# Optimization experiments

Measured on AMD Instinct MI355X. Metric: run time of the kernel, lower is better.

Reference implementation:

```python
import jax, jax.numpy as jnp
import numpy as np

B, S, HID, NH = 2, 2048, 1024, 16
HD = HID // NH
SCALE = HD ** -0.5


def elu_plus_one(x):
    return jax.nn.elu(x) + 1.0


def setup_inputs() -> dict:
    key = jax.random.key(0)
    ks = jax.random.split(key, 8)
    w_scale = 0.02  # keep logits in a sane range
    return {
        "hidden_states": jax.random.normal(ks[0], (B, S, HID), jnp.float32),
        "wq": jax.random.normal(ks[1], (HID, HID), jnp.float32) * w_scale,
        "wk": jax.random.normal(ks[2], (HID, HID), jnp.float32) * w_scale,
        "wv": jax.random.normal(ks[3], (HID, HID), jnp.float32) * w_scale,
        "wo": jax.random.normal(ks[4], (HID, HID), jnp.float32) * w_scale,
        "beta": jax.random.normal(ks[5], (NH,), jnp.float32),
        "memory": jax.random.normal(ks[6], (NH, HD, HD), jnp.float32),
        "memory_norm": jax.random.uniform(ks[7], (NH, HD), jnp.float32),
    }


def reference(hidden_states, wq, wk, wv, wo, beta, memory, memory_norm):
    b, s, _ = hidden_states.shape
    # nn.Linear(bias=False): x @ W^T; weights stored [out, in]
    def proj(x, w):
        return jnp.einsum("bsh,oh->bso", x, w).reshape(b, s, NH, HD).transpose(0, 2, 1, 3)

    q = proj(hidden_states, wq)  # [B,H,S,D]
    k = proj(hidden_states, wk)
    v = proj(hidden_states, wv)

    # local causal softmax attention (materializes [B,H,S,S] as the original does)
    scores = jnp.einsum("bhsd,bhtd->bhst", q, k) * SCALE
    causal_mask = jnp.triu(jnp.full((s, s), -jnp.inf, dtype=scores.dtype), k=1)
    attn = jax.nn.softmax(scores + causal_mask, axis=-1)
    a_local = jnp.einsum("bhst,bhtd->bhsd", attn, v)

    # compressive memory retrieval: sigma(Q) @ M / (sigma(Q) @ z)
    sigma_q = elu_plus_one(q)
    a_mem_unnorm = jnp.einsum("bhsd,hde->bhse", sigma_q, memory)
    norm = jnp.clip(jnp.einsum("bhsd,hd->bhs", sigma_q, memory_norm), 1e-6, None)
    a_mem = a_mem_unnorm / norm[..., None]

    gate = jax.nn.sigmoid(beta).reshape(1, NH, 1, 1)
    combined = gate * a_mem + (1.0 - gate) * a_local  # [B,H,S,D]
    combined = combined.transpose(0, 2, 1, 3).reshape(b, s, HID)
    return jnp.einsum("bsh,oh->bso", combined, wo)
```

## Files before the change

kernel.cpp:

```cpp
#include <hip/hip_runtime.h>
#include <stdint.h>

#define LOG2E 1.4426950408889634f

typedef __attribute__((ext_vector_type(8))) __bf16 bf16x8;
typedef __attribute__((ext_vector_type(4))) __bf16 bf16x4;
typedef __attribute__((ext_vector_type(4))) float f32x4;

__device__ inline void gll16(const void* g, void* l) {
  __builtin_amdgcn_global_load_lds(
      (const __attribute__((address_space(1))) void*)g,
      (__attribute__((address_space(3))) void*)l, 16, 0, 0);
}

__global__ __launch_bounds__(256) void cvt_all(
    const float* __restrict__ hs, const float* __restrict__ wq,
    const float* __restrict__ wk, const float* __restrict__ wv,
    const float* __restrict__ wo,
    __bf16* __restrict__ hsb, __bf16* __restrict__ wqb, __bf16* __restrict__ wkb,
    __bf16* __restrict__ wvb, __bf16* __restrict__ wob) {
  int bid = blockIdx.x;
  const float* s; __bf16* d; int i;
  if (bid < 4096) { s = hs; d = hsb; i = bid * 256 + threadIdx.x; }
  else {
    int seg = (bid - 4096) >> 10;
    i = ((bid - 4096) & 1023) * 256 + threadIdx.x;
    s = seg == 0 ? wq : seg == 1 ? wk : seg == 2 ? wv : wo;
    d = seg == 0 ? wqb : seg == 1 ? wkb : seg == 2 ? wvb : wob;
  }
  float4 v = ((const float4*)s)[i];
  bf16x4 o;
  o[0] = (__bf16)v.x; o[1] = (__bf16)v.y; o[2] = (__bf16)v.z; o[3] = (__bf16)v.w;
  *(bf16x4*)&d[(size_t)i * 4] = o;
}

#define KSCALE 0.18033688011112042f
__global__ __launch_bounds__(256, 3) void qkv_gemm(
    const __bf16* __restrict__ hsb, const __bf16* __restrict__ wqb,
    const __bf16* __restrict__ wkb, const __bf16* __restrict__ wvb,
    __bf16* __restrict__ qbuf, __bf16* __restrict__ kbuf,
    __bf16* __restrict__ vtb) {
  constexpr int K = 1024;
  __shared__ __align__(16) __bf16 lta[128 * 32];
  __shared__ __align__(16) __bf16 ltb[128 * 32];
  const int bid = blockIdx.x;
  const int z = bid >> 8, r = bid & 255;
  const __bf16 *A, *Bt;
  int m0, n0;
  if (z < 2) {
    A = hsb; Bt = z ? wkb : wqb;
    m0 = (r & 31) * 128; n0 = (r >> 5) * 128;
  } else {
    A = wvb; Bt = hsb;
    m0 = (r & 7) * 128; n0 = (r >> 3) * 128;
  }
  const int tid = threadIdx.x;
  const int w = tid >> 6, l = tid & 63;
  const int lg = l >> 4, lr = l & 15;
  const int wm = (w >> 1) * 64, wn = (w & 1) * 64;
  f32x4 acc[4][4] = {};
  const int srow = w * 16 + (l >> 2);
  const int scol = (l & 3) * 8;
  const __bf16* ga = A + (size_t)(m0 + srow) * K + scol;
  const __bf16* gb = Bt + (size_t)(n0 + srow) * K + scol;
  __bf16* la = &lta[(size_t)w * 16 * 32];
  __bf16* lb = &ltb[(size_t)w * 16 * 32];
  for (int k0 = 0; k0 < K; k0 += 32) {
    __syncthreads();
    gll16(ga + k0, la);
    gll16(ga + 64 * K + k0, la + 64 * 32);
    gll16(gb + k0, lb);
    gll16(gb + 64 * K + k0, lb + 64 * 32);
    __syncthreads();
    bf16x8 af[4], bfr[4];
#pragma unroll
    for (int i = 0; i < 4; ++i) {
      af[i]  = *(const bf16x8*)&lta[(wm + i * 16 + lr) * 32 + lg * 8];
      bfr[i] = *(const bf16x8*)&ltb[(wn + i * 16 + lr) * 32 + lg * 8];
    }
#pragma unroll
    for (int i = 0; i < 4; ++i)
#pragma unroll
      for (int j = 0; j < 4; ++j)
        acc[i][j] = __builtin_amdgcn_mfma_f32_16x16x32_bf16(af[i], bfr[j], acc[i][j], 0, 0, 0);
  }
#pragma unroll
  for (int i = 0; i < 4; ++i)
#pragma unroll
    for (int j = 0; j < 4; ++j)
#pragma unroll
      for (int rr = 0; rr < 4; ++rr) {
        int gm = m0 + wm + i * 16 + lg * 4 + rr;
        int gn = n0 + wn + j * 16 + lr;
        float v = acc[i][j][rr];
        if (z < 2) {
          int bb = gm >> 11, s = gm & 2047, hh = gn >> 6, d = gn & 63;
          __bf16* dst = z ? kbuf : qbuf;
          if (z) v *= KSCALE;
          dst[(((size_t)bb * 16 + hh) * 2048 + s) * 64 + d] = (__bf16)v;
        } else {
          int bb = gn >> 11, s = gn & 2047, hh = gm >> 6, d = gm & 63;
          vtb[(((size_t)bb * 16 + hh) * 64 + d) * 2048 + s] = (__bf16)v;
        }
      }
}

__global__ __launch_bounds__(256, 2) void gemm_out(const __bf16* __restrict__ A,
                                                   const __bf16* __restrict__ Bt,
                                                   float* __restrict__ C,
                                                   int M, int N) {
  constexpr int K = 1024;
  __shared__ __align__(16) __bf16 lta[128 * 32];
  __shared__ __align__(16) __bf16 ltb[64 * 32];
  const int tid = threadIdx.x;
  const int w = tid >> 6, l = tid & 63;
  const int lg = l >> 4, lr = l & 15;
  const int m0 = blockIdx.x * 128, n0 = blockIdx.y * 64;
  const int wm = (w >> 1) * 64, wn = (w & 1) * 32;
  f32x4 acc[4][2] = {};
  const int srow = tid >> 2;
  const int scol = (tid & 3) * 8;
  const __bf16* ga = A + (size_t)(m0 + srow) * K + scol;
  const __bf16* gb = Bt + (size_t)(n0 + srow) * K + scol;
  __bf16* la = &lta[(size_t)w * 512];
  __bf16* lb = &ltb[(size_t)w * 512];
  for (int k0 = 0; k0 < K; k0 += 32) {
    __syncthreads();
    gll16(ga + k0, la);
    gll16(ga + (size_t)64 * K + k0, la + 64 * 32);
    gll16(gb + k0, lb);
    __syncthreads();
    bf16x8 af[4], bfr[2];
#pragma unroll
    for (int i = 0; i < 4; ++i)
      af[i]  = *(const bf16x8*)&lta[(wm + i * 16 + lr) * 32 + lg * 8];
#pragma unroll
    for (int j = 0; j < 2; ++j)
      bfr[j] = *(const bf16x8*)&ltb[(wn + j * 16 + lr) * 32 + lg * 8];
#pragma unroll
    for (int i = 0; i < 4; ++i)
#pragma unroll
      for (int j = 0; j < 2; ++j)
        acc[i][j] = __builtin_amdgcn_mfma_f32_16x16x32_bf16(af[i], bfr[j], acc[i][j], 0, 0, 0);
  }
#pragma unroll
  for (int i = 0; i < 4; ++i)
#pragma unroll
    for (int j = 0; j < 2; ++j)
#pragma unroll
      for (int rr = 0; rr < 4; ++rr) {
        int gm = m0 + wm + i * 16 + lg * 4 + rr;
        int gn = n0 + wn + j * 16 + lr;
        C[(size_t)gm * N + gn] = acc[i][j][rr];
      }
}

#define DEFER_THR 11.5f
#define SWZ(row, col) (((row) << 7) + ((col) ^ (((row) & 7) << 3)))
#define SWZK(row, col) (((row) << 6) + ((col) ^ (((row) & 7) << 3)))

__global__ __launch_bounds__(256, 2) void attn_kernel(
    const __bf16* __restrict__ qb,
    const __bf16* __restrict__ kb,
    const __bf16* __restrict__ vtb,
    const float* __restrict__ memory,
    const float* __restrict__ memnorm,
    const float* __restrict__ beta,
    __bf16* __restrict__ comb)
{
  __shared__ __align__(16) __bf16 kt[2][128 * 64];
  __shared__ __align__(16) __bf16 vt[2][64 * 128];
  __shared__ __align__(16) __bf16 pt[4][16 * 128];

  const int tid = threadIdx.x;
  const int w = tid >> 6, l = tid & 63;
  const int lg = l >> 4, lr = l & 15;
  const int qh = w & 1, par = w >> 1;
  const int ltid = tid & 127;
  const int t = 31 - (blockIdx.x >> 5);
  const int bh = blockIdx.x & 31;
  const int hh = bh & 15, b = bh >> 4;
  const int wq0 = t * 64 + qh * 32;
  const int nt = (t >> 1) + 1;
  const int cA = (nt + 1) >> 1;
  const int cnt = par ? (nt - cA) : cA;
  const int kvbase = par ? cA * 128 : 0;

  const int s_sk = ltid >> 3, s_d8 = (ltid & 7) * 8;
  const int s_d = ltid >> 4, s_sk8 = (ltid & 15) * 8;
  const __bf16* kbase = kb + ((size_t)bh * 2048 + kvbase + s_sk) * 64 + s_d8;
  const __bf16* vbase = vtb + ((size_t)bh * 64 + s_d) * 2048 + kvbase + s_sk8;

  bf16x8 qf[2][2];
#pragma unroll
  for (int mf = 0; mf < 2; ++mf)
#pragma unroll
    for (int kk = 0; kk < 2; ++kk)
      qf[mf][kk] = *(const bf16x8*)(qb + ((size_t)bh * 2048 + wq0 + mf * 16 + lr) * 64 + kk * 32 + lg * 8);

  bf16x8 kst[8], vst[8];
  if (cnt > 0) {
#pragma unroll
    for (int i = 0; i < 8; ++i) {
      kst[i] = *(const bf16x8*)(kbase + i * 1024);
      vst[i] = *(const bf16x8*)(vbase + (size_t)i * 16384);
    }
  }

  float mrun[2] = {-1e30f, -1e30f}, lsum[2] = {0.f, 0.f};
  f32x4 apv[2][4] = {};

  for (int kv = 0; kv < cA; ++kv) {
    const bool vcur = kv < cnt;
    __syncthreads();
    if (vcur) {
#pragma unroll
      for (int i = 0; i < 8; ++i) {
        *(bf16x8*)&kt[par][SWZK(s_sk + i * 16, s_d8)] = kst[i];
        *(bf16x8*)&vt[par][SWZ(s_d + i * 8, s_sk8)] = vst[i];
      }
    }
    __syncthreads();
    if (kv + 1 < cnt) {
#pragma unroll
      for (int i = 0; i < 8; ++i) {
        kst[i] = *(const bf16x8*)(kbase + (size_t)(kv + 1) * 8192 + i * 1024);
        vst[i] = *(const bf16x8*)(vbase + (kv + 1) * 128 + (size_t)i * 16384);
      }
    }
    if (!vcur) continue;
    const int kv0 = kvbase + kv * 128;

    f32x4 sc[2][8] = {};
#pragma unroll
    for (int kk = 0; kk < 2; ++kk)
#pragma unroll
      for (int nf = 0; nf < 8; ++nf) {
        bf16x8 kf = *(const bf16x8*)&kt[par][SWZK(nf * 16 + lr, kk * 32 + lg * 8)];
#pragma unroll
        for (int mf = 0; mf < 2; ++mf)
          sc[mf][nf] = __builtin_amdgcn_mfma_f32_16x16x32_bf16(kf, qf[mf][kk], sc[mf][nf], 0, 0, 0);
      }

    if (kv0 + 127 > wq0) {
#pragma unroll
      for (int mf = 0; mf < 2; ++mf) {
        const int qrow = wq0 + mf * 16 + lr;
#pragma unroll
        for (int nf = 0; nf < 8; ++nf)
#pragma unroll
          for (int r = 0; r < 4; ++r)
            if (kv0 + nf * 16 + lg * 4 + r > qrow) sc[mf][nf][r] = -1e30f;
      }
    }

#pragma unroll
    for (int mf = 0; mf < 2; ++mf) {
      f32x4 m4 = sc[mf][0];
#pragma unroll
      for (int nf = 1; nf < 8; ++nf)
#pragma unroll
        for (int r = 0; r < 4; ++r) m4[r] = fmaxf(m4[r], sc[mf][nf][r]);
      float mx = fmaxf(fmaxf(m4[0], m4[1]), fmaxf(m4[2], m4[3]));
      mx = fmaxf(mx, __shfl_xor(mx, 16, 64));
      mx = fmaxf(mx, __shfl_xor(mx, 32, 64));
      if (!__all(mx - mrun[mf] <= DEFER_THR)) {
        float mold = mrun[mf];
        float mn = fmaxf(mold, mx);
        mrun[mf] = mn;
        float scl = __builtin_amdgcn_exp2f(mold - mn);
        lsum[mf] *= scl;
        float sclq[4];
#pragma unroll
        for (int r = 0; r < 4; ++r) sclq[r] = __shfl(scl, (lg << 2) | r, 16);
#pragma unroll
        for (int nf = 0; nf < 4; ++nf)
#pragma unroll
          for (int r = 0; r < 4; ++r) apv[mf][nf][r] *= sclq[r];
      }
    }

    bf16x8 pa0[4];
    {
      float rs = 0.f;
#pragma unroll
      for (int nf = 0; nf < 8; ++nf) {
        bf16x4 pk;
#pragma unroll
        for (int r = 0; r < 4; ++r) {
          float pv = __builtin_amdgcn_exp2f(sc[0][nf][r] - mrun[0]);
          rs += pv;
          pk[r] = (__bf16)pv;
        }
        *(bf16x4*)&pt[w][SWZ(lr, nf * 16 + lg * 4)] = pk;
      }
      rs += __shfl_xor(rs, 16, 64);
      rs += __shfl_xor(rs, 32, 64);
      lsum[0] += rs;
#pragma unroll
      for (int kk = 0; kk < 4; ++kk)
        pa0[kk] = *(const bf16x8*)&pt[w][SWZ(lr, kk * 32 + lg * 8)];
    }
    {
      float rs = 0.f;
#pragma unroll
      for (int nf = 0; nf < 8; ++nf) {
        bf16x4 pk;
#pragma unroll
        for (int r = 0; r < 4; ++r) {
          float pv = __builtin_amdgcn_exp2f(sc[1][nf][r] - mrun[1]);
          rs += pv;
          pk[r] = (__bf16)pv;
        }
        *(bf16x4*)&pt[w][SWZ(lr, nf * 16 + lg * 4)] = pk;
      }
      rs += __shfl_xor(rs, 16, 64);
      rs += __shfl_xor(rs, 32, 64);
      lsum[1] += rs;
    }

#pragma unroll
    for (int kk = 0; kk < 4; ++kk) {
      bf16x8 pa1 = *(const bf16x8*)&pt[w][SWZ(lr, kk * 32 + lg * 8)];
#pragma unroll
      for (int nf = 0; nf < 4; ++nf) {
        bf16x8 vf = *(const bf16x8*)&vt[par][SWZ(nf * 16 + lr, kk * 32 + lg * 8)];
        apv[0][nf] = __builtin_amdgcn_mfma_f32_16x16x32_bf16(pa0[kk], vf, apv[0][nf], 0, 0, 0);
        apv[1][nf] = __builtin_amdgcn_mfma_f32_16x16x32_bf16(pa1, vf, apv[1][nf], 0, 0, 0);
      }
    }
  }

  __syncthreads();
  float* dumpO  = (float*)&kt[0][0];
  float* dumpML = (float*)&vt[0][0];
  __bf16* mt = &kt[1][0];
  if (par == 1) {
#pragma unroll
    for (int mf = 0; mf < 2; ++mf) {
#pragma unroll
      for (int nf = 0; nf < 4; ++nf)
#pragma unroll
        for (int r = 0; r < 4; ++r)
          dumpO[qh * 2048 + (mf * 16 + lg * 4 + r) * 64 + nf * 16 + lr] = apv[mf][nf][r];
      dumpML[qh * 64 + mf * 16 + lr] = mrun[mf];
      dumpML[128 + qh * 64 + mf * 16 + lr] = lsum[mf];
    }
  } else {
    for (int i = tid; i < 64 * 64; i += 128) {
      int d = i >> 6, e = i & 63;
      mt[e * 72 + d] = (__bf16)memory[((size_t)hh * 64 + d) * 64 + e];
    }
    for (int i = tid; i < 16 * 64; i += 128) {
      int e = 64 + (i >> 6), d = i & 63;
      mt[e * 72 + d] = (__bf16)memnorm[hh * 64 + d];
    }
  }
  __syncthreads();
  if (par == 1) return;

  float lq[2][4], f1v[2], f2v[2];
#pragma unroll
  for (int mf = 0; mf < 2; ++mf) {
    float m2 = dumpML[qh * 64 + mf * 16 + lr];
    float l2 = dumpML[128 + qh * 64 + mf * 16 + lr];
    float m1 = mrun[mf];
    float fm = fmaxf(m1, m2);
    f1v[mf] = __builtin_amdgcn_exp2f(m1 - fm);
    f2v[mf] = __builtin_amdgcn_exp2f(m2 - fm);
    float lm = f1v[mf] * lsum[mf] + f2v[mf] * l2;
#pragma unroll
    for (int r = 0; r < 4; ++r) lq[mf][r] = __shfl(lm, (lg << 2) | r, 16);
  }
#pragma unroll
  for (int mf = 0; mf < 2; ++mf)
#pragma unroll
    for (int r = 0; r < 4; ++r) {
      float f1q = __shfl(f1v[mf], (lg << 2) | r, 16);
      float f2q = __shfl(f2v[mf], (lg << 2) | r, 16);
#pragma unroll
      for (int nf = 0; nf < 4; ++nf) {
        float o2 = dumpO[qh * 2048 + (mf * 16 + lg * 4 + r) * 64 + nf * 16 + lr];
        apv[mf][nf][r] = f1q * apv[mf][nf][r] + f2q * o2;
      }
    }

  bf16x8 sf[2][2];
#pragma unroll
  for (int mf = 0; mf < 2; ++mf)
#pragma unroll
    for (int kk = 0; kk < 2; ++kk) {
      bf16x8 q = qf[mf][kk], s;
#pragma unroll
      for (int j = 0; j < 8; ++j) {
        float x = (float)q[j];
        float sg = x > 0.f ? x + 1.f : __builtin_amdgcn_exp2f(x * LOG2E);
        s[j] = (__bf16)sg;
      }
      sf[mf][kk] = s;
    }
  f32x4 am[2][5] = {};
#pragma unroll
  for (int kk = 0; kk < 2; ++kk)
#pragma unroll
    for (int nf = 0; nf < 5; ++nf) {
      bf16x8 bb = *(const bf16x8*)&mt[(nf * 16 + lr) * 72 + kk * 32 + lg * 8];
#pragma unroll
      for (int mf = 0; mf < 2; ++mf)
        am[mf][nf] = __builtin_amdgcn_mfma_f32_16x16x32_bf16(sf[mf][kk], bb, am[mf][nf], 0, 0, 0);
    }

  const float gate = 1.f / (1.f + __builtin_amdgcn_exp2f(-beta[hh] * LOG2E));
  const float og = 1.f - gate;
#pragma unroll
  for (int mf = 0; mf < 2; ++mf)
#pragma unroll
    for (int r = 0; r < 4; ++r) {
      int row = wq0 + mf * 16 + lg * 4 + r;
      float linv = __builtin_amdgcn_rcpf(lq[mf][r]);
      float nrm = fmaxf(am[mf][4][r], 1e-6f);
      float ninv = __builtin_amdgcn_rcpf(nrm);
      size_t base = ((size_t)b * 2048 + row) * 1024 + hh * 64;
#pragma unroll
      for (int nf = 0; nf < 4; ++nf)
        comb[base + nf * 16 + lr] =
            (__bf16)(gate * am[mf][nf][r] * ninv + og * apv[mf][nf][r] * linv);
    }
}

extern "C" void kernel_launch(void* const* d_in, const int* in_sizes, int n_in,
                              void* d_out, int out_size, void* d_ws, size_t ws_size,
                              hipStream_t stream) {
  const float* hs      = (const float*)d_in[0];
  const float* wq      = (const float*)d_in[1];
  const float* wk      = (const float*)d_in[2];
  const float* wv      = (const float*)d_in[3];
  const float* wo      = (const float*)d_in[4];
  const float* beta    = (const float*)d_in[5];
  const float* memory  = (const float*)d_in[6];
  const float* memnorm = (const float*)d_in[7];
  float* out = (float*)d_out;

  char* ws = (char*)d_ws;
  __bf16* hsb  = (__bf16*)(ws);
  __bf16* wqb  = (__bf16*)(ws + ((size_t)8  << 20));
  __bf16* wkb  = (__bf16*)(ws + ((size_t)10 << 20));
  __bf16* wvb  = (__bf16*)(ws + ((size_t)12 << 20));
  __bf16* wob  = (__bf16*)(ws + ((size_t)14 << 20));
  __bf16* qbuf = (__bf16*)(ws + ((size_t)16 << 20));
  __bf16* kbuf = (__bf16*)(ws + ((size_t)24 << 20));
  __bf16* vtb  = (__bf16*)(ws + ((size_t)32 << 20));
  __bf16* comb = (__bf16*)(ws + ((size_t)40 << 20));

  cvt_all<<<8192, 256, 0, stream>>>(hs, wq, wk, wv, wo, hsb, wqb, wkb, wvb, wob);

  qkv_gemm<<<768, 256, 0, stream>>>(hsb, wqb, wkb, wvb, qbuf, kbuf, vtb);

  attn_kernel<<<1024, 256, 0, stream>>>(qbuf, kbuf, vtb, memory, memnorm, beta, comb);

  gemm_out<<<dim3(32, 16), 256, 0, stream>>>(comb, wob, out, 4096, 1024);
}
```

Before: 114.4 us.

## Replace split-KV attention with 128-row query tiles and direct global-to-LDS loads

The attention kernel no longer splits each query tile's KV range between two wave pairs and merges partial softmax states. Each block now covers 128 query rows with four waves sharing every KV tile, and K/V tiles are loaded straight into LDS with pre-swizzled global_load_lds instead of being staged through registers. The grid is halved and the tile order is changed to interleave long and short causal tiles. This drops the merge pass and the register prefetch, and each loaded KV tile feeds twice as many queries. In exchange the kernel loses its software prefetch overlap, since each load sits between barriers, and there are fewer blocks to fill the GPU.

New measurement: 110.4 us. 1.04x faster.

```diff
diff --git a/kernel.cpp b/kernel.cpp
--- a/kernel.cpp
+++ b/kernel.cpp
@@ -168,28 +168,28 @@
     const float* __restrict__ beta,
     __bf16* __restrict__ comb)
 {
-  __shared__ __align__(16) __bf16 kt[2][128 * 64];
-  __shared__ __align__(16) __bf16 vt[2][64 * 128];
+  __shared__ __align__(16) __bf16 kt[128 * 64];
+  __shared__ __align__(16) __bf16 vt[64 * 128];
   __shared__ __align__(16) __bf16 pt[4][16 * 128];
 
   const int tid = threadIdx.x;
   const int w = tid >> 6, l = tid & 63;
   const int lg = l >> 4, lr = l & 15;
-  const int qh = w & 1, par = w >> 1;
-  const int ltid = tid & 127;
-  const int t = 31 - (blockIdx.x >> 5);
+  const int tt = blockIdx.x >> 5;
+  const int t = (tt < 8) ? (15 - tt) : (tt - 8);
   const int bh = blockIdx.x & 31;
   const int hh = bh & 15, b = bh >> 4;
-  const int wq0 = t * 64 + qh * 32;
-  const int nt = (t >> 1) + 1;
-  const int cA = (nt + 1) >> 1;
-  const int cnt = par ? (nt - cA) : cA;
-  const int kvbase = par ? cA * 128 : 0;
-
-  const int s_sk = ltid >> 3, s_d8 = (ltid & 7) * 8;
-  const int s_d = ltid >> 4, s_sk8 = (ltid & 15) * 8;
-  const __bf16* kbase = kb + ((size_t)bh * 2048 + kvbase + s_sk) * 64 + s_d8;
-  const __bf16* vbase = vtb + ((size_t)bh * 64 + s_d) * 2048 + kvbase + s_sk8;
+  const int wq0 = t * 128 + w * 32;
+  const int ntiles = t + 1;
+
+  const int k_row = tid >> 3;
+  const int k_col = ((tid & 7) ^ (k_row & 7)) * 8;
+  const __bf16* ksrc = kb + ((size_t)bh * 2048 + k_row) * 64 + k_col;
+  const int v_d = tid >> 4;
+  const int v_col = ((tid & 15) ^ (v_d & 7)) * 8;
+  const __bf16* vsrc = vtb + ((size_t)bh * 64 + v_d) * 2048 + v_col;
+  __bf16* kdst = &kt[w * 512];
+  __bf16* vdst = &vt[w * 512];
 
   bf16x8 qf[2][2];
 #pragma unroll
@@ -198,51 +198,31 @@
     for (int kk = 0; kk < 2; ++kk)
       qf[mf][kk] = *(const bf16x8*)(qb + ((size_t)bh * 2048 + wq0 + mf * 16 + lr) * 64 + kk * 32 + lg * 8);
 
-  bf16x8 kst[8], vst[8];
-  if (cnt > 0) {
-#pragma unroll
-    for (int i = 0; i < 8; ++i) {
-      kst[i] = *(const bf16x8*)(kbase + i * 1024);
-      vst[i] = *(const bf16x8*)(vbase + (size_t)i * 16384);
-    }
-  }
-
   float mrun[2] = {-1e30f, -1e30f}, lsum[2] = {0.f, 0.f};
   f32x4 apv[2][4] = {};
 
-  for (int kv = 0; kv < cA; ++kv) {
-    const bool vcur = kv < cnt;
-    __syncthreads();
-    if (vcur) {
-#pragma unroll
-      for (int i = 0; i < 8; ++i) {
-        *(bf16x8*)&kt[par][SWZK(s_sk + i * 16, s_d8)] = kst[i];
-        *(bf16x8*)&vt[par][SWZ(s_d + i * 8, s_sk8)] = vst[i];
-      }
-    }
-    __syncthreads();
-    if (kv + 1 < cnt) {
-#pragma unroll
-      for (int i = 0; i < 8; ++i) {
-        kst[i] = *(const bf16x8*)(kbase + (size_t)(kv + 1) * 8192 + i * 1024);
-        vst[i] = *(const bf16x8*)(vbase + (kv + 1) * 128 + (size_t)i * 16384);
-      }
-    }
-    if (!vcur) continue;
-    const int kv0 = kvbase + kv * 128;
+  for (int kv = 0; kv < ntiles; ++kv) {
+    const int kv0 = kv * 128;
+    __syncthreads();
+#pragma unroll
+    for (int i = 0; i < 4; ++i) {
+      gll16(ksrc + (size_t)(kv0 + i * 32) * 64, kdst + i * 2048);
+      gll16(vsrc + (size_t)i * 16 * 2048 + kv0, vdst + i * 2048);
+    }
+    __syncthreads();
 
     f32x4 sc[2][8] = {};
 #pragma unroll
     for (int kk = 0; kk < 2; ++kk)
 #pragma unroll
       for (int nf = 0; nf < 8; ++nf) {
-        bf16x8 kf = *(const bf16x8*)&kt[par][SWZK(nf * 16 + lr, kk * 32 + lg * 8)];
+        bf16x8 kf = *(const bf16x8*)&kt[SWZK(nf * 16 + lr, kk * 32 + lg * 8)];
 #pragma unroll
         for (int mf = 0; mf < 2; ++mf)
           sc[mf][nf] = __builtin_amdgcn_mfma_f32_16x16x32_bf16(kf, qf[mf][kk], sc[mf][nf], 0, 0, 0);
       }
 
-    if (kv0 + 127 > wq0) {
+    if (kv == ntiles - 1) {
 #pragma unroll
       for (int mf = 0; mf < 2; ++mf) {
         const int qrow = wq0 + mf * 16 + lr;
@@ -324,7 +304,7 @@
       bf16x8 pa1 = *(const bf16x8*)&pt[w][SWZ(lr, kk * 32 + lg * 8)];
 #pragma unroll
       for (int nf = 0; nf < 4; ++nf) {
-        bf16x8 vf = *(const bf16x8*)&vt[par][SWZ(nf * 16 + lr, kk * 32 + lg * 8)];
+        bf16x8 vf = *(const bf16x8*)&vt[SWZ(nf * 16 + lr, kk * 32 + lg * 8)];
         apv[0][nf] = __builtin_amdgcn_mfma_f32_16x16x32_bf16(pa0[kk], vf, apv[0][nf], 0, 0, 0);
         apv[1][nf] = __builtin_amdgcn_mfma_f32_16x16x32_bf16(pa1, vf, apv[1][nf], 0, 0, 0);
       }
@@ -332,58 +312,16 @@
   }
 
   __syncthreads();
-  float* dumpO  = (float*)&kt[0][0];
-  float* dumpML = (float*)&vt[0][0];
-  __bf16* mt = &kt[1][0];
-  if (par == 1) {
-#pragma unroll
-    for (int mf = 0; mf < 2; ++mf) {
-#pragma unroll
-      for (int nf = 0; nf < 4; ++nf)
-#pragma unroll
-        for (int r = 0; r < 4; ++r)
-          dumpO[qh * 2048 + (mf * 16 + lg * 4 + r) * 64 + nf * 16 + lr] = apv[mf][nf][r];
-      dumpML[qh * 64 + mf * 16 + lr] = mrun[mf];
-      dumpML[128 + qh * 64 + mf * 16 + lr] = lsum[mf];
-    }
-  } else {
-    for (int i = tid; i < 64 * 64; i += 128) {
-      int d = i >> 6, e = i & 63;
-      mt[e * 72 + d] = (__bf16)memory[((size_t)hh * 64 + d) * 64 + e];
-    }
-    for (int i = tid; i < 16 * 64; i += 128) {
-      int e = 64 + (i >> 6), d = i & 63;
-      mt[e * 72 + d] = (__bf16)memnorm[hh * 64 + d];
-    }
+  __bf16* mt = kt;
+  for (int i = tid; i < 64 * 64; i += 256) {
+    int d = i >> 6, e = i & 63;
+    mt[e * 72 + d] = (__bf16)memory[((size_t)hh * 64 + d) * 64 + e];
+  }
+  for (int i = tid; i < 16 * 64; i += 256) {
+    int e = 64 + (i >> 6), d = i & 63;
+    mt[e * 72 + d] = (__bf16)memnorm[hh * 64 + d];
   }
   __syncthreads();
-  if (par == 1) return;
-
-  float lq[2][4], f1v[2], f2v[2];
-#pragma unroll
-  for (int mf = 0; mf < 2; ++mf) {
-    float m2 = dumpML[qh * 64 + mf * 16 + lr];
-    float l2 = dumpML[128 + qh * 64 + mf * 16 + lr];
-    float m1 = mrun[mf];
-    float fm = fmaxf(m1, m2);
-    f1v[mf] = __builtin_amdgcn_exp2f(m1 - fm);
-    f2v[mf] = __builtin_amdgcn_exp2f(m2 - fm);
-    float lm = f1v[mf] * lsum[mf] + f2v[mf] * l2;
-#pragma unroll
-    for (int r = 0; r < 4; ++r) lq[mf][r] = __shfl(lm, (lg << 2) | r, 16);
-  }
-#pragma unroll
-  for (int mf = 0; mf < 2; ++mf)
-#pragma unroll
-    for (int r = 0; r < 4; ++r) {
-      float f1q = __shfl(f1v[mf], (lg << 2) | r, 16);
-      float f2q = __shfl(f2v[mf], (lg << 2) | r, 16);
-#pragma unroll
-      for (int nf = 0; nf < 4; ++nf) {
-        float o2 = dumpO[qh * 2048 + (mf * 16 + lg * 4 + r) * 64 + nf * 16 + lr];
-        apv[mf][nf][r] = f1q * apv[mf][nf][r] + f2q * o2;
-      }
-    }
 
   bf16x8 sf[2][2];
 #pragma unroll
@@ -399,6 +337,7 @@
       }
       sf[mf][kk] = s;
     }
+
   f32x4 am[2][5] = {};
 #pragma unroll
   for (int kk = 0; kk < 2; ++kk)
@@ -413,11 +352,14 @@
   const float gate = 1.f / (1.f + __builtin_amdgcn_exp2f(-beta[hh] * LOG2E));
   const float og = 1.f - gate;
 #pragma unroll
-  for (int mf = 0; mf < 2; ++mf)
+  for (int mf = 0; mf < 2; ++mf) {
+    float lsq[4];
+#pragma unroll
+    for (int r = 0; r < 4; ++r) lsq[r] = __shfl(lsum[mf], (lg << 2) | r, 16);
 #pragma unroll
     for (int r = 0; r < 4; ++r) {
       int row = wq0 + mf * 16 + lg * 4 + r;
-      float linv = __builtin_amdgcn_rcpf(lq[mf][r]);
+      float linv = __builtin_amdgcn_rcpf(lsq[r]);
       float nrm = fmaxf(am[mf][4][r], 1e-6f);
       float ninv = __builtin_amdgcn_rcpf(nrm);
       size_t base = ((size_t)b * 2048 + row) * 1024 + hh * 64;
@@ -426,6 +368,7 @@
         comb[base + nf * 16 + lr] =
             (__bf16)(gate * am[mf][nf][r] * ninv + og * apv[mf][nf][r] * linv);
     }
+  }
 }
 
 extern "C" void kernel_launch(void* const* d_in, const int* in_sizes, int n_in,
@@ -456,7 +399,7 @@
 
   qkv_gemm<<<768, 256, 0, stream>>>(hsb, wqb, wkb, wvb, qbuf, kbuf, vtb);
 
-  attn_kernel<<<1024, 256, 0, stream>>>(qbuf, kbuf, vtb, memory, memnorm, beta, comb);
+  attn_kernel<<<512, 256, 0, stream>>>(qbuf, kbuf, vtb, memory, memnorm, beta, comb);
 
   gemm_out<<<dim3(32, 16), 256, 0, stream>>>(comb, wob, out, 4096, 1024);
 }
```

## Pair causal query tiles per block, shrink KV tiles, use direct global-to-LDS loads

Applied to the files above, without the earlier changes.

The attention kernel now processes two query tiles per block (tile p and its mirror 31-p), which balances the causal workload and halves the grid. KV tiles drop from 128 to 64 keys, and staging goes through global_load_lds instead of register prefetch, cutting LDS use so launch bounds can target 4 blocks per CU. The memory matrix load is vectorised with float4. In exchange, the register-level prefetch double buffering is gone, so the loads are no longer overlapped with compute and each tile iteration pays two barriers, while shorter tiles also mean more loop iterations.

Result: slower. 122.2 us (+6.8%).

```diff
diff --git a/kernel.cpp b/kernel.cpp
--- a/kernel.cpp
+++ b/kernel.cpp
@@ -156,10 +156,9 @@
 }
 
 #define DEFER_THR 11.5f
-#define SWZ(row, col) (((row) << 7) + ((col) ^ (((row) & 7) << 3)))
-#define SWZK(row, col) (((row) << 6) + ((col) ^ (((row) & 7) << 3)))
-
-__global__ __launch_bounds__(256, 2) void attn_kernel(
+#define SWZ64(row, col) (((row) << 6) + ((col) ^ (((row) & 7) << 3)))
+
+__global__ __launch_bounds__(256, 4) void attn_kernel(
     const __bf16* __restrict__ qb,
     const __bf16* __restrict__ kb,
     const __bf16* __restrict__ vtb,
@@ -168,264 +167,263 @@
     const float* __restrict__ beta,
     __bf16* __restrict__ comb)
 {
-  __shared__ __align__(16) __bf16 kt[2][128 * 64];
-  __shared__ __align__(16) __bf16 vt[2][64 * 128];
-  __shared__ __align__(16) __bf16 pt[4][16 * 128];
+  __shared__ __align__(16) __bf16 kt[2][64 * 64];
+  __shared__ __align__(16) __bf16 vt[2][64 * 64];
+  __shared__ __align__(16) __bf16 pt[4][16 * 64];
 
   const int tid = threadIdx.x;
   const int w = tid >> 6, l = tid & 63;
   const int lg = l >> 4, lr = l & 15;
   const int qh = w & 1, par = w >> 1;
-  const int ltid = tid & 127;
-  const int t = 31 - (blockIdx.x >> 5);
+  const int p = blockIdx.x >> 5;
   const int bh = blockIdx.x & 31;
   const int hh = bh & 15, b = bh >> 4;
-  const int wq0 = t * 64 + qh * 32;
-  const int nt = (t >> 1) + 1;
-  const int cA = (nt + 1) >> 1;
-  const int cnt = par ? (nt - cA) : cA;
-  const int kvbase = par ? cA * 128 : 0;
-
-  const int s_sk = ltid >> 3, s_d8 = (ltid & 7) * 8;
-  const int s_d = ltid >> 4, s_sk8 = (ltid & 15) * 8;
-  const __bf16* kbase = kb + ((size_t)bh * 2048 + kvbase + s_sk) * 64 + s_d8;
-  const __bf16* vbase = vtb + ((size_t)bh * 64 + s_d) * 2048 + kvbase + s_sk8;
-
-  bf16x8 qf[2][2];
-#pragma unroll
-  for (int mf = 0; mf < 2; ++mf)
-#pragma unroll
-    for (int kk = 0; kk < 2; ++kk)
-      qf[mf][kk] = *(const bf16x8*)(qb + ((size_t)bh * 2048 + wq0 + mf * 16 + lr) * 64 + kk * 32 + lg * 8);
-
-  bf16x8 kst[8], vst[8];
-  if (cnt > 0) {
-#pragma unroll
-    for (int i = 0; i < 8; ++i) {
-      kst[i] = *(const bf16x8*)(kbase + i * 1024);
-      vst[i] = *(const bf16x8*)(vbase + (size_t)i * 16384);
-    }
-  }
-
-  float mrun[2] = {-1e30f, -1e30f}, lsum[2] = {0.f, 0.f};
-  f32x4 apv[2][4] = {};
-
-  for (int kv = 0; kv < cA; ++kv) {
-    const bool vcur = kv < cnt;
-    __syncthreads();
-    if (vcur) {
-#pragma unroll
-      for (int i = 0; i < 8; ++i) {
-        *(bf16x8*)&kt[par][SWZK(s_sk + i * 16, s_d8)] = kst[i];
-        *(bf16x8*)&vt[par][SWZ(s_d + i * 8, s_sk8)] = vst[i];
-      }
-    }
-    __syncthreads();
-    if (kv + 1 < cnt) {
-#pragma unroll
-      for (int i = 0; i < 8; ++i) {
-        kst[i] = *(const bf16x8*)(kbase + (size_t)(kv + 1) * 8192 + i * 1024);
-        vst[i] = *(const bf16x8*)(vbase + (kv + 1) * 128 + (size_t)i * 16384);
-      }
-    }
-    if (!vcur) continue;
-    const int kv0 = kvbase + kv * 128;
-
-    f32x4 sc[2][8] = {};
-#pragma unroll
-    for (int kk = 0; kk < 2; ++kk)
-#pragma unroll
-      for (int nf = 0; nf < 8; ++nf) {
-        bf16x8 kf = *(const bf16x8*)&kt[par][SWZK(nf * 16 + lr, kk * 32 + lg * 8)];
-#pragma unroll
-        for (int mf = 0; mf < 2; ++mf)
-          sc[mf][nf] = __builtin_amdgcn_mfma_f32_16x16x32_bf16(kf, qf[mf][kk], sc[mf][nf], 0, 0, 0);
-      }
-
-    if (kv0 + 127 > wq0) {
-#pragma unroll
-      for (int mf = 0; mf < 2; ++mf) {
-        const int qrow = wq0 + mf * 16 + lr;
-#pragma unroll
-        for (int nf = 0; nf < 8; ++nf)
-#pragma unroll
-          for (int r = 0; r < 4; ++r)
-            if (kv0 + nf * 16 + lg * 4 + r > qrow) sc[mf][nf][r] = -1e30f;
-      }
-    }
-
-#pragma unroll
-    for (int mf = 0; mf < 2; ++mf) {
-      f32x4 m4 = sc[mf][0];
-#pragma unroll
-      for (int nf = 1; nf < 8; ++nf)
-#pragma unroll
-        for (int r = 0; r < 4; ++r) m4[r] = fmaxf(m4[r], sc[mf][nf][r]);
-      float mx = fmaxf(fmaxf(m4[0], m4[1]), fmaxf(m4[2], m4[3]));
-      mx = fmaxf(mx, __shfl_xor(mx, 16, 64));
-      mx = fmaxf(mx, __shfl_xor(mx, 32, 64));
-      if (!__all(mx - mrun[mf] <= DEFER_THR)) {
-        float mold = mrun[mf];
-        float mn = fmaxf(mold, mx);
-        mrun[mf] = mn;
-        float scl = __builtin_amdgcn_exp2f(mold - mn);
-        lsum[mf] *= scl;
-        float sclq[4];
-#pragma unroll
-        for (int r = 0; r < 4; ++r) sclq[r] = __shfl(scl, (lg << 2) | r, 16);
-#pragma unroll
-        for (int nf = 0; nf < 4; ++nf)
-#pragma unroll
-          for (int r = 0; r < 4; ++r) apv[mf][nf][r] *= sclq[r];
-      }
-    }
-
-    bf16x8 pa0[4];
-    {
-      float rs = 0.f;
-#pragma unroll
-      for (int nf = 0; nf < 8; ++nf) {
-        bf16x4 pk;
-#pragma unroll
-        for (int r = 0; r < 4; ++r) {
-          float pv = __builtin_amdgcn_exp2f(sc[0][nf][r] - mrun[0]);
-          rs += pv;
-          pk[r] = (__bf16)pv;
-        }
-        *(bf16x4*)&pt[w][SWZ(lr, nf * 16 + lg * 4)] = pk;
-      }
-      rs += __shfl_xor(rs, 16, 64);
-      rs += __shfl_xor(rs, 32, 64);
-      lsum[0] += rs;
-#pragma unroll
-      for (int kk = 0; kk < 4; ++kk)
-        pa0[kk] = *(const bf16x8*)&pt[w][SWZ(lr, kk * 32 + lg * 8)];
-    }
-    {
-      float rs = 0.f;
-#pragma unroll
-      for (int nf = 0; nf < 8; ++nf) {
-        bf16x4 pk;
-#pragma unroll
-        for (int r = 0; r < 4; ++r) {
-          float pv = __builtin_amdgcn_exp2f(sc[1][nf][r] - mrun[1]);
-          rs += pv;
-          pk[r] = (__bf16)pv;
-        }
-        *(bf16x4*)&pt[w][SWZ(lr, nf * 16 + lg * 4)] = pk;
-      }
-      rs += __shfl_xor(rs, 16, 64);
-      rs += __shfl_xor(rs, 32, 64);
-      lsum[1] += rs;
-    }
-
-#pragma unroll
-    for (int kk = 0; kk < 4; ++kk) {
-      bf16x8 pa1 = *(const bf16x8*)&pt[w][SWZ(lr, kk * 32 + lg * 8)];
-#pragma unroll
-      for (int nf = 0; nf < 4; ++nf) {
-        bf16x8 vf = *(const bf16x8*)&vt[par][SWZ(nf * 16 + lr, kk * 32 + lg * 8)];
-        apv[0][nf] = __builtin_amdgcn_mfma_f32_16x16x32_bf16(pa0[kk], vf, apv[0][nf], 0, 0, 0);
-        apv[1][nf] = __builtin_amdgcn_mfma_f32_16x16x32_bf16(pa1, vf, apv[1][nf], 0, 0, 0);
-      }
-    }
-  }
-
-  __syncthreads();
-  float* dumpO  = (float*)&kt[0][0];
-  float* dumpML = (float*)&vt[0][0];
-  __bf16* mt = &kt[1][0];
-  if (par == 1) {
-#pragma unroll
-    for (int mf = 0; mf < 2; ++mf) {
-#pragma unroll
-      for (int nf = 0; nf < 4; ++nf)
-#pragma unroll
-        for (int r = 0; r < 4; ++r)
-          dumpO[qh * 2048 + (mf * 16 + lg * 4 + r) * 64 + nf * 16 + lr] = apv[mf][nf][r];
-      dumpML[qh * 64 + mf * 16 + lr] = mrun[mf];
-      dumpML[128 + qh * 64 + mf * 16 + lr] = lsum[mf];
-    }
-  } else {
-    for (int i = tid; i < 64 * 64; i += 128) {
-      int d = i >> 6, e = i & 63;
-      mt[e * 72 + d] = (__bf16)memory[((size_t)hh * 64 + d) * 64 + e];
-    }
-    for (int i = tid; i < 16 * 64; i += 128) {
-      int e = 64 + (i >> 6), d = i & 63;
-      mt[e * 72 + d] = (__bf16)memnorm[hh * 64 + d];
-    }
-  }
-  __syncthreads();
-  if (par == 1) return;
-
-  float lq[2][4], f1v[2], f2v[2];
-#pragma unroll
-  for (int mf = 0; mf < 2; ++mf) {
-    float m2 = dumpML[qh * 64 + mf * 16 + lr];
-    float l2 = dumpML[128 + qh * 64 + mf * 16 + lr];
-    float m1 = mrun[mf];
-    float fm = fmaxf(m1, m2);
-    f1v[mf] = __builtin_amdgcn_exp2f(m1 - fm);
-    f2v[mf] = __builtin_amdgcn_exp2f(m2 - fm);
-    float lm = f1v[mf] * lsum[mf] + f2v[mf] * l2;
-#pragma unroll
-    for (int r = 0; r < 4; ++r) lq[mf][r] = __shfl(lm, (lg << 2) | r, 16);
-  }
-#pragma unroll
-  for (int mf = 0; mf < 2; ++mf)
-#pragma unroll
-    for (int r = 0; r < 4; ++r) {
-      float f1q = __shfl(f1v[mf], (lg << 2) | r, 16);
-      float f2q = __shfl(f2v[mf], (lg << 2) | r, 16);
-#pragma unroll
-      for (int nf = 0; nf < 4; ++nf) {
-        float o2 = dumpO[qh * 2048 + (mf * 16 + lg * 4 + r) * 64 + nf * 16 + lr];
-        apv[mf][nf][r] = f1q * apv[mf][nf][r] + f2q * o2;
-      }
-    }
-
-  bf16x8 sf[2][2];
-#pragma unroll
-  for (int mf = 0; mf < 2; ++mf)
-#pragma unroll
-    for (int kk = 0; kk < 2; ++kk) {
-      bf16x8 q = qf[mf][kk], s;
-#pragma unroll
-      for (int j = 0; j < 8; ++j) {
-        float x = (float)q[j];
-        float sg = x > 0.f ? x + 1.f : __builtin_amdgcn_exp2f(x * LOG2E);
-        s[j] = (__bf16)sg;
-      }
-      sf[mf][kk] = s;
-    }
-  f32x4 am[2][5] = {};
-#pragma unroll
-  for (int kk = 0; kk < 2; ++kk)
-#pragma unroll
-    for (int nf = 0; nf < 5; ++nf) {
-      bf16x8 bb = *(const bf16x8*)&mt[(nf * 16 + lr) * 72 + kk * 32 + lg * 8];
-#pragma unroll
-      for (int mf = 0; mf < 2; ++mf)
-        am[mf][nf] = __builtin_amdgcn_mfma_f32_16x16x32_bf16(sf[mf][kk], bb, am[mf][nf], 0, 0, 0);
-    }
 
   const float gate = 1.f / (1.f + __builtin_amdgcn_exp2f(-beta[hh] * LOG2E));
   const float og = 1.f - gate;
-#pragma unroll
-  for (int mf = 0; mf < 2; ++mf)
-#pragma unroll
-    for (int r = 0; r < 4; ++r) {
-      int row = wq0 + mf * 16 + lg * 4 + r;
-      float linv = __builtin_amdgcn_rcpf(lq[mf][r]);
-      float nrm = fmaxf(am[mf][4][r], 1e-6f);
-      float ninv = __builtin_amdgcn_rcpf(nrm);
-      size_t base = ((size_t)b * 2048 + row) * 1024 + hh * 64;
-#pragma unroll
-      for (int nf = 0; nf < 4; ++nf)
-        comb[base + nf * 16 + lr] =
-            (__bf16)(gate * am[mf][nf][r] * ninv + og * apv[mf][nf][r] * linv);
+
+  const int srw = qh * 8 + (l >> 3);
+  const int c8 = ((l & 7) ^ (l >> 3)) * 8;
+  const __bf16* kbase = kb + ((size_t)bh * 2048 + srw) * 64 + c8;
+  const __bf16* vbase = vtb + ((size_t)bh * 64 + srw) * 2048 + c8;
+
+  for (int phase = 0; phase < 2; ++phase) {
+    const int ti = phase ? (31 - p) : p;
+    const int wq0 = ti * 64 + qh * 32;
+    const int ntk = ti + 1;
+    const int cA = (ntk + 1) >> 1;
+    const int cnt = par ? (ntk - cA) : cA;
+    const int kvg0 = par ? cA : 0;
+
+    bf16x8 qf[2][2];
+#pragma unroll
+    for (int mf = 0; mf < 2; ++mf)
+#pragma unroll
+      for (int kk = 0; kk < 2; ++kk)
+        qf[mf][kk] = *(const bf16x8*)(qb + ((size_t)bh * 2048 + wq0 + mf * 16 + lr) * 64 + kk * 32 + lg * 8);
+
+    float mrun[2] = {-1e30f, -1e30f}, lsum[2] = {0.f, 0.f};
+    f32x4 apv[2][4] = {};
+
+    for (int kv = 0; kv < cA; ++kv) {
+      const bool vcur = kv < cnt;
+      const int kvg = kvg0 + kv;
+      __syncthreads();
+      if (vcur) {
+#pragma unroll
+        for (int i = 0; i < 4; ++i) {
+          gll16(kbase + (size_t)kvg * 4096 + i * 1024, &kt[par][i * 1024 + qh * 512]);
+          gll16(vbase + (size_t)i * 32768 + kvg * 64, &vt[par][i * 1024 + qh * 512]);
+        }
+      }
+      __syncthreads();
+      if (!vcur) continue;
+      const int kv0 = kvg * 64;
+
+      f32x4 sc[2][4] = {};
+#pragma unroll
+      for (int kk = 0; kk < 2; ++kk)
+#pragma unroll
+        for (int nf = 0; nf < 4; ++nf) {
+          bf16x8 kf = *(const bf16x8*)&kt[par][SWZ64(nf * 16 + lr, kk * 32 + lg * 8)];
+#pragma unroll
+          for (int mf = 0; mf < 2; ++mf)
+            sc[mf][nf] = __builtin_amdgcn_mfma_f32_16x16x32_bf16(kf, qf[mf][kk], sc[mf][nf], 0, 0, 0);
+        }
+
+      if (kv0 + 63 > wq0) {
+#pragma unroll
+        for (int mf = 0; mf < 2; ++mf) {
+          const int qrow = wq0 + mf * 16 + lr;
+#pragma unroll
+          for (int nf = 0; nf < 4; ++nf)
+#pragma unroll
+            for (int r = 0; r < 4; ++r)
+              if (kv0 + nf * 16 + lg * 4 + r > qrow) sc[mf][nf][r] = -1e30f;
+        }
+      }
+
+#pragma unroll
+      for (int mf = 0; mf < 2; ++mf) {
+        f32x4 m4 = sc[mf][0];
+#pragma unroll
+        for (int nf = 1; nf < 4; ++nf)
+#pragma unroll
+          for (int r = 0; r < 4; ++r) m4[r] = fmaxf(m4[r], sc[mf][nf][r]);
+        float mx = fmaxf(fmaxf(m4[0], m4[1]), fmaxf(m4[2], m4[3]));
+        mx = fmaxf(mx, __shfl_xor(mx, 16, 64));
+        mx = fmaxf(mx, __shfl_xor(mx, 32, 64));
+        if (!__all(mx - mrun[mf] <= DEFER_THR)) {
+          float mold = mrun[mf];
+          float mn = fmaxf(mold, mx);
+          mrun[mf] = mn;
+          float scl = __builtin_amdgcn_exp2f(mold - mn);
+          lsum[mf] *= scl;
+          float sclq[4];
+#pragma unroll
+          for (int r = 0; r < 4; ++r) sclq[r] = __shfl(scl, (lg << 2) | r, 16);
+#pragma unroll
+          for (int nf = 0; nf < 4; ++nf)
+#pragma unroll
+            for (int r = 0; r < 4; ++r) apv[mf][nf][r] *= sclq[r];
+        }
+      }
+
+      bf16x8 pa0[2];
+      {
+        f32x4 rs4 = {0.f, 0.f, 0.f, 0.f};
+#pragma unroll
+        for (int nf = 0; nf < 4; ++nf) {
+          bf16x4 pk;
+#pragma unroll
+          for (int r = 0; r < 4; ++r) {
+            float pv = __builtin_amdgcn_exp2f(sc[0][nf][r] - mrun[0]);
+            rs4[r] += pv;
+            pk[r] = (__bf16)pv;
+          }
+          *(bf16x4*)&pt[w][SWZ64(lr, nf * 16 + lg * 4)] = pk;
+        }
+        float rs = (rs4[0] + rs4[1]) + (rs4[2] + rs4[3]);
+        rs += __shfl_xor(rs, 16, 64);
+        rs += __shfl_xor(rs, 32, 64);
+        lsum[0] += rs;
+#pragma unroll
+        for (int kk = 0; kk < 2; ++kk)
+          pa0[kk] = *(const bf16x8*)&pt[w][SWZ64(lr, kk * 32 + lg * 8)];
+      }
+      {
+        f32x4 rs4 = {0.f, 0.f, 0.f, 0.f};
+#pragma unroll
+        for (int nf = 0; nf < 4; ++nf) {
+          bf16x4 pk;
+#pragma unroll
+          for (int r = 0; r < 4; ++r) {
+            float pv = __builtin_amdgcn_exp2f(sc[1][nf][r] - mrun[1]);
+            rs4[r] += pv;
+            pk[r] = (__bf16)pv;
+          }
+          *(bf16x4*)&pt[w][SWZ64(lr, nf * 16 + lg * 4)] = pk;
+        }
+        float rs = (rs4[0] + rs4[1]) + (rs4[2] + rs4[3]);
+        rs += __shfl_xor(rs, 16, 64);
+        rs += __shfl_xor(rs, 32, 64);
+        lsum[1] += rs;
+      }
+
+#pragma unroll
+      for (int kk = 0; kk < 2; ++kk) {
+        bf16x8 pa1 = *(const bf16x8*)&pt[w][SWZ64(lr, kk * 32 + lg * 8)];
+#pragma unroll
+        for (int nf = 0; nf < 4; ++nf) {
+          bf16x8 vf = *(const bf16x8*)&vt[par][SWZ64(nf * 16 + lr, kk * 32 + lg * 8)];
+          apv[0][nf] = __builtin_amdgcn_mfma_f32_16x16x32_bf16(pa0[kk], vf, apv[0][nf], 0, 0, 0);
+          apv[1][nf] = __builtin_amdgcn_mfma_f32_16x16x32_bf16(pa1, vf, apv[1][nf], 0, 0, 0);
+        }
+      }
     }
+
+    __syncthreads();
+    float* dumpO  = (float*)&kt[0][0];
+    __bf16* mt    = &vt[0][0];
+    float* dumpML = (float*)((char*)&vt[0][0] + 11520);
+    if (par == 1) {
+#pragma unroll
+      for (int mf = 0; mf < 2; ++mf) {
+#pragma unroll
+        for (int nf = 0; nf < 4; ++nf)
+#pragma unroll
+          for (int r = 0; r < 4; ++r)
+            dumpO[(qh * 32 + mf * 16 + lg * 4 + r) * 64 + nf * 16 + lr] = apv[mf][nf][r];
+        dumpML[qh * 32 + mf * 16 + lr] = mrun[mf];
+        dumpML[64 + qh * 32 + mf * 16 + lr] = lsum[mf];
+      }
+    } else {
+      const int lt = tid;
+      for (int i4 = lt; i4 < 1024; i4 += 128) {
+        int d = i4 >> 4, e0 = (i4 & 15) * 4;
+        float4 mv = *(const float4*)&memory[((size_t)hh * 64 + d) * 64 + e0];
+        mt[(e0 + 0) * 72 + d] = (__bf16)mv.x;
+        mt[(e0 + 1) * 72 + d] = (__bf16)mv.y;
+        mt[(e0 + 2) * 72 + d] = (__bf16)mv.z;
+        mt[(e0 + 3) * 72 + d] = (__bf16)mv.w;
+      }
+      for (int i = lt; i < 1024; i += 128) {
+        int e = 64 + (i >> 6), d = i & 63;
+        mt[e * 72 + d] = (__bf16)memnorm[hh * 64 + d];
+      }
+    }
+    __syncthreads();
+
+    if (par == 0) {
+      float lq[2][4], f1v[2], f2v[2];
+#pragma unroll
+      for (int mf = 0; mf < 2; ++mf) {
+        float m2 = dumpML[qh * 32 + mf * 16 + lr];
+        float l2 = dumpML[64 + qh * 32 + mf * 16 + lr];
+        float m1 = mrun[mf];
+        float fm = fmaxf(m1, m2);
+        f1v[mf] = __builtin_amdgcn_exp2f(m1 - fm);
+        f2v[mf] = __builtin_amdgcn_exp2f(m2 - fm);
+        float lm = f1v[mf] * lsum[mf] + f2v[mf] * l2;
+#pragma unroll
+        for (int r = 0; r < 4; ++r) lq[mf][r] = __shfl(lm, (lg << 2) | r, 16);
+      }
+#pragma unroll
+      for (int mf = 0; mf < 2; ++mf)
+#pragma unroll
+        for (int r = 0; r < 4; ++r) {
+          float f1q = __shfl(f1v[mf], (lg << 2) | r, 16);
+          float f2q = __shfl(f2v[mf], (lg << 2) | r, 16);
+#pragma unroll
+          for (int nf = 0; nf < 4; ++nf) {
+            float o2 = dumpO[(qh * 32 + mf * 16 + lg * 4 + r) * 64 + nf * 16 + lr];
+            apv[mf][nf][r] = f1q * apv[mf][nf][r] + f2q * o2;
+          }
+        }
+
+      bf16x8 sf[2][2];
+#pragma unroll
+      for (int mf = 0; mf < 2; ++mf)
+#pragma unroll
+        for (int kk = 0; kk < 2; ++kk) {
+          bf16x8 q = qf[mf][kk], s;
+#pragma unroll
+          for (int j = 0; j < 8; ++j) {
+            float x = (float)q[j];
+            float sg = x > 0.f ? x + 1.f : __builtin_amdgcn_exp2f(x * LOG2E);
+            s[j] = (__bf16)sg;
+          }
+          sf[mf][kk] = s;
+        }
+      f32x4 am[2][5] = {};
+#pragma unroll
+      for (int kk = 0; kk < 2; ++kk)
+#pragma unroll
+        for (int nf = 0; nf < 5; ++nf) {
+          bf16x8 bb = *(const bf16x8*)&mt[(nf * 16 + lr) * 72 + kk * 32 + lg * 8];
+#pragma unroll
+          for (int mf = 0; mf < 2; ++mf)
+            am[mf][nf] = __builtin_amdgcn_mfma_f32_16x16x32_bf16(sf[mf][kk], bb, am[mf][nf], 0, 0, 0);
+        }
+
+#pragma unroll
+      for (int mf = 0; mf < 2; ++mf) {
+#pragma unroll
+        for (int r = 0; r < 4; ++r) {
+          int row = wq0 + mf * 16 + lg * 4 + r;
+          float linv = __builtin_amdgcn_rcpf(lq[mf][r]);
+          float nrm = fmaxf(am[mf][4][r], 1e-6f);
+          float ninv = __builtin_amdgcn_rcpf(nrm);
+          size_t base = ((size_t)b * 2048 + row) * 1024 + hh * 64;
+#pragma unroll
+          for (int nf = 0; nf < 4; ++nf)
+            comb[base + nf * 16 + lr] =
+                (__bf16)(gate * am[mf][nf][r] * ninv + og * apv[mf][nf][r] * linv);
+        }
+      }
+    }
+    __syncthreads();
+  }
 }
 
 extern "C" void kernel_launch(void* const* d_in, const int* in_sizes, int n_in,
@@ -456,7 +454,7 @@
 
   qkv_gemm<<<768, 256, 0, stream>>>(hsb, wqb, wkb, wvb, qbuf, kbuf, vtb);
 
-  attn_kernel<<<1024, 256, 0, stream>>>(qbuf, kbuf, vtb, memory, memnorm, beta, comb);
+  attn_kernel<<<512, 256, 0, stream>>>(qbuf, kbuf, vtb, memory, memnorm, beta, comb);
 
   gemm_out<<<dim3(32, 16), 256, 0, stream>>>(comb, wob, out, 4096, 1024);
 }
```
